# Kernel optimization log

Measured on AMD Instinct MI355X. Metric: run time of the kernel, lower is better.

Reference implementation:

```python
import jax, jax.numpy as jnp
import numpy as np

N_NODES = 50000


def _gcn_conv(x, src, dst, W, b, num_nodes):
    """PyG GCNConv: out = D^{-1/2}(A+I)D^{-1/2} (x @ W) + b, self-loops added."""
    h = x @ W  # [N, out]
    # degrees over edges incl. self-loops (src/dst already include self-loops)
    ones = jnp.ones(src.shape[0], dtype=h.dtype)
    deg = jax.ops.segment_sum(ones, dst, num_segments=num_nodes)
    dinv = jnp.where(deg > 0, jax.lax.rsqrt(deg), 0.0)
    norm = dinv[src] * dinv[dst]  # [E]
    msgs = h[src] * norm[:, None]  # [E, out] gather (memory-bound)
    out = jax.ops.segment_sum(msgs, dst, num_segments=num_nodes)
    return out + b


def setup_inputs() -> dict:
    key = jax.random.key(0)
    ks = jax.random.split(key, 8)
    in_c, h2, h1, out_c = 256, 256, 128, 128
    x = jax.random.normal(ks[0], (N_NODES, in_c), dtype=jnp.float32)
    edge_index = jax.random.randint(ks[1], (2, 800000), 0, N_NODES, dtype=jnp.int64)
    def glorot(k, fi, fo):
        s = float(np.sqrt(6.0 / (fi + fo)))
        return jax.random.uniform(k, (fi, fo), jnp.float32, -s, s)
    return {
        "x": x,
        "edge_index": edge_index,
        "W1": glorot(ks[2], in_c, h2), "b1": jnp.zeros((h2,), jnp.float32),
        "W2": glorot(ks[3], h2, h1), "b2": jnp.zeros((h1,), jnp.float32),
        "W3": glorot(ks[4], h1, out_c), "b3": jnp.zeros((out_c,), jnp.float32),
    }


def reference(x, edge_index, W1, b1, W2, b2, W3, b3):
    n = x.shape[0]
    loops = jnp.arange(n, dtype=edge_index.dtype)
    src = jnp.concatenate([edge_index[0], loops])
    dst = jnp.concatenate([edge_index[1], loops])
    # dropout is a no-op in eval mode (training=False)
    h1 = jax.nn.relu(_gcn_conv(x, src, dst, W1, b1, n))
    h2 = jax.nn.relu(_gcn_conv(h1, src, dst, W2, b2, n))
    h3 = jax.nn.relu(_gcn_conv(h2, src, dst, W3, b3, n))
    return jnp.concatenate([h1, h2, h3], axis=1)
```

## Files before the change

### kernel.cpp

```cpp
#include <hip/hip_runtime.h>

typedef __attribute__((ext_vector_type(8))) short bfrag8;
typedef __attribute__((ext_vector_type(4))) float f32x4v;

__device__ inline short f2bf(float f) {
    unsigned u = __builtin_bit_cast(unsigned, f);
    u = (u + 0x7FFFu + ((u >> 16) & 1u)) >> 16;
    return (short)u;
}
__device__ inline float bf2f(short s) {
    unsigned u = ((unsigned)(unsigned short)s) << 16;
    return __builtin_bit_cast(float, u);
}
__device__ inline int pack2(short lo, short hi) {
    return (int)(((unsigned)(unsigned short)lo) | (((unsigned)(unsigned short)hi) << 16));
}
__device__ inline void gload_lds16(const short* g, short* l) {
    __builtin_amdgcn_global_load_lds(
        (const __attribute__((address_space(1))) void*)g,
        (__attribute__((address_space(3))) void*)l, 16, 0, 0);
}


__global__ void deg_count_kernel(const int* __restrict__ dst, int E, int* __restrict__ deg) {
    int e = blockIdx.x * blockDim.x + threadIdx.x;
    if (e < E) atomicAdd(&deg[dst[e]], 1);
}

__global__ void block_sum_kernel(const int* __restrict__ deg, int n, int* __restrict__ bsums) {
    int i = blockIdx.x * 256 + threadIdx.x;
    int v = (i < n) ? deg[i] : 0;
#pragma unroll
    for (int off = 32; off > 0; off >>= 1) v += __shfl_down(v, off);
    __shared__ int wsum[4];
    int lane = threadIdx.x & 63, w = threadIdx.x >> 6;
    if (lane == 0) wsum[w] = v;
    __syncthreads();
    if (threadIdx.x == 0) bsums[blockIdx.x] = wsum[0] + wsum[1] + wsum[2] + wsum[3];
}

__global__ void scan_bsums_kernel(int* __restrict__ bsums, int B, int* __restrict__ offs, int n) {
    __shared__ int s[256];
    int tid = threadIdx.x;
    int v = (tid < B) ? bsums[tid] : 0;
    s[tid] = v;
    __syncthreads();
    for (int off = 1; off < 256; off <<= 1) {
        int t = (tid >= off) ? s[tid - off] : 0;
        __syncthreads();
        s[tid] += t;
        __syncthreads();
    }
    if (tid < B) bsums[tid] = (tid == 0) ? 0 : s[tid - 1];
    if (tid == 0) offs[n] = s[255];
}

__global__ void scan_final_kernel(const int* __restrict__ deg, int n,
                                  const int* __restrict__ bsums,
                                  int* __restrict__ offs, int* __restrict__ cursor,
                                  float* __restrict__ dinv) {
    __shared__ int s[256];
    int tid = threadIdx.x;
    int i = blockIdx.x * 256 + tid;
    int v = (i < n) ? deg[i] : 0;
    s[tid] = v;
    __syncthreads();
    for (int off = 1; off < 256; off <<= 1) {
        int t = (tid >= off) ? s[tid - off] : 0;
        __syncthreads();
        s[tid] += t;
        __syncthreads();
    }
    if (i < n) {
        int excl = s[tid] - v + bsums[blockIdx.x];
        offs[i] = excl;
        cursor[i] = excl;
        dinv[i] = rsqrtf((float)(v + 1));
    }
}

__global__ void csr_fill_kernel(const int* __restrict__ src, const int* __restrict__ dst, int E,
                                int* __restrict__ cursor, int* __restrict__ csr) {
    int e = blockIdx.x * blockDim.x + threadIdx.x;
    if (e < E) {
        int d = dst[e];
        int p = atomicAdd(&cursor[d], 1);
        csr[p] = src[e];
    }
}


__global__ void wt_kernel(const float* __restrict__ W, short* __restrict__ Wt,
                          int K, int logN) {
    int i = blockIdx.x * blockDim.x + threadIdx.x;
    int total = K << logN;
    if (i < total) {
        int k = i >> logN;
        int n = i & ((1 << logN) - 1);
        Wt[(size_t)n * K + k] = f2bf(W[i]);
    }
}


__global__ void x2b_kernel(const float* __restrict__ x, short* __restrict__ xb, int total8) {
    int i = blockIdx.x * blockDim.x + threadIdx.x;
    if (i < total8) {
        const float4* p = (const float4*)(x + (size_t)i * 8);
        float4 v0 = p[0], v1 = p[1];
        int4 w = make_int4(pack2(f2bf(v0.x), f2bf(v0.y)), pack2(f2bf(v0.z), f2bf(v0.w)),
                           pack2(f2bf(v1.x), f2bf(v1.y)), pack2(f2bf(v1.z), f2bf(v1.w)));
        *(int4*)(xb + (size_t)i * 8) = w;
    }
}


__global__ __launch_bounds__(256) void gemm_bf16_kernel(
        const short* __restrict__ A, int lda,
        const short* __restrict__ Bt, int K,
        const float* __restrict__ dinv,
        short* __restrict__ Tout, int ldt,
        int M) {
    __shared__ short As[128 * 32];
    __shared__ short Bs[128 * 32];

    const int tid = threadIdx.x;
    const int lane = tid & 63;
    const int wid = tid >> 6;
    const int l15 = lane & 15;
    const int quad = lane >> 4;
    const int q8 = quad * 8;
    const int bm = blockIdx.x * 128;
    const int bn = blockIdx.y * 128;
    const int wm = (wid & 1) * 64;
    const int wn = (wid >> 1) * 64;

    f32x4v acc[4][4];
#pragma unroll
    for (int i = 0; i < 4; ++i)
#pragma unroll
        for (int j = 0; j < 4; ++j) acc[i][j] = (f32x4v){0.f, 0.f, 0.f, 0.f};

    const int f0 = wid * 2048 + lane * 16;
    const int r0 = f0 >> 6, c0 = (f0 & 63) >> 1;
    const int f1 = f0 + 1024;
    const int r1 = f1 >> 6, c1 = (f1 & 63) >> 1;
    short* ldsA = As + wid * 1024;
    short* ldsB = Bs + wid * 1024;

    const short* a0 = A + (size_t)(bm + r0) * lda + c0;
    const short* a1 = A + (size_t)(bm + r1) * lda + c1;
    const short* b0 = Bt + (size_t)(bn + r0) * K + c0;
    const short* b1 = Bt + (size_t)(bn + r1) * K + c1;

    for (int k0 = 0; k0 < K; k0 += 32) {
        gload_lds16(a0 + k0, ldsA);
        gload_lds16(a1 + k0, ldsA + 512);
        gload_lds16(b0 + k0, ldsB);
        gload_lds16(b1 + k0, ldsB + 512);
        __syncthreads();

        bfrag8 af[4], bfv[4];
#pragma unroll
        for (int mt = 0; mt < 4; ++mt)
            af[mt] = *(const bfrag8*)&As[(wm + mt * 16 + l15) * 32 + q8];
#pragma unroll
        for (int nt = 0; nt < 4; ++nt)
            bfv[nt] = *(const bfrag8*)&Bs[(wn + nt * 16 + l15) * 32 + q8];
#pragma unroll
        for (int mt = 0; mt < 4; ++mt)
#pragma unroll
            for (int nt = 0; nt < 4; ++nt)
                acc[mt][nt] = __builtin_amdgcn_mfma_f32_16x16x32_bf16(af[mt], bfv[nt], acc[mt][nt], 0, 0, 0);
        __syncthreads();
    }

#pragma unroll
    for (int mt = 0; mt < 4; ++mt) {
#pragma unroll
        for (int r = 0; r < 4; ++r) {
            int grow = bm + wm + mt * 16 + quad * 4 + r;
            if (grow < M) {
                float di = dinv[grow];
                short* outp = Tout + (size_t)grow * ldt + bn + wn + l15;
#pragma unroll
                for (int nt = 0; nt < 4; ++nt)
                    outp[nt * 16] = f2bf(acc[mt][nt][r] * di);
            }
        }
    }
}


template<int C, bool WB>
__global__ __launch_bounds__(256) void agg_kernel(
        const short* __restrict__ hn, const float* __restrict__ dinv,
        const int* __restrict__ offs, const int* __restrict__ csr,
        const float* __restrict__ bias, float* __restrict__ out,
        short* __restrict__ hb, int coloff, int n) {
    constexpr int V = C / 64;
    int node = blockIdx.x * 4 + (threadIdx.x >> 6);
    if (node >= n) return;
    int lane = threadIdx.x & 63;
    const short* base = hn + lane * V;

    float acc[V];
#pragma unroll
    for (int v = 0; v < V; ++v) acc[v] = 0.f;

    int beg = offs[node], end = offs[node + 1];
    int e = beg;
    if (V == 4) {
        for (; e + 8 <= end; e += 8) {
            short4 r[8];
#pragma unroll
            for (int j = 0; j < 8; ++j)
                r[j] = *(const short4*)(base + (size_t)csr[e + j] * C);
#pragma unroll
            for (int j = 0; j < 8; ++j) {
                acc[0] += bf2f(r[j].x); acc[1] += bf2f(r[j].y);
                acc[2] += bf2f(r[j].z); acc[3] += bf2f(r[j].w);
            }
        }
        for (; e < end; ++e) {
            short4 a = *(const short4*)(base + (size_t)csr[e] * C);
            acc[0] += bf2f(a.x); acc[1] += bf2f(a.y); acc[2] += bf2f(a.z); acc[3] += bf2f(a.w);
        }
        short4 a = *(const short4*)(base + (size_t)node * C);
        acc[0] += bf2f(a.x); acc[1] += bf2f(a.y); acc[2] += bf2f(a.z); acc[3] += bf2f(a.w);
    } else {
        for (; e + 8 <= end; e += 8) {
            short2 r[8];
#pragma unroll
            for (int j = 0; j < 8; ++j)
                r[j] = *(const short2*)(base + (size_t)csr[e + j] * C);
#pragma unroll
            for (int j = 0; j < 8; ++j) {
                acc[0] += bf2f(r[j].x); acc[1] += bf2f(r[j].y);
            }
        }
        for (; e < end; ++e) {
            short2 a = *(const short2*)(base + (size_t)csr[e] * C);
            acc[0] += bf2f(a.x); acc[1] += bf2f(a.y);
        }
        short2 a = *(const short2*)(base + (size_t)node * C);
        acc[0] += bf2f(a.x); acc[1] += bf2f(a.y);
    }

    float di = dinv[node];
    float res[V];
#pragma unroll
    for (int v = 0; v < V; ++v)
        res[v] = fmaxf(fmaf(di, acc[v], bias[lane * V + v]), 0.f);

    float* op = out + (size_t)node * 512 + coloff + lane * V;
    if (V == 4) {
        *(float4*)op = make_float4(res[0], res[1], res[2], res[3]);
        if (WB) {
            int2 w = make_int2(pack2(f2bf(res[0]), f2bf(res[1])), pack2(f2bf(res[2]), f2bf(res[3])));
            *(int2*)(hb + (size_t)node * C + lane * V) = w;
        }
    } else {
        *(float2*)op = make_float2(res[0], res[1]);
        if (WB) {
            *(int*)(hb + (size_t)node * C + lane * V) = pack2(f2bf(res[0]), f2bf(res[1]));
        }
    }
}


extern "C" void kernel_launch(void* const* d_in, const int* in_sizes, int n_in,
                              void* d_out, int out_size, void* d_ws, size_t ws_size,
                              hipStream_t stream) {
    const float* x  = (const float*)d_in[0];
    const int*   ei = (const int*)d_in[1];
    const float* W1 = (const float*)d_in[2];
    const float* b1 = (const float*)d_in[3];
    const float* W2 = (const float*)d_in[4];
    const float* b2 = (const float*)d_in[5];
    const float* W3 = (const float*)d_in[6];
    const float* b3 = (const float*)d_in[7];

    const int IN_C = 256, H2 = 256, H1 = 128, OUT_C = 128;
    int n = in_sizes[0] / IN_C;
    int E = in_sizes[1] / 2;
    const int* src = ei;
    const int* dst = ei + E;

    int mb = (n + 127) / 128;
    int npad = mb * 128;

    char* ws = (char*)d_ws;
    auto carve = [&](size_t bytes) { char* p = ws; ws += (bytes + 255) & ~(size_t)255; return p; };
    int*   deg    = (int*)  carve((size_t)n * 4);
    int*   offs   = (int*)  carve(((size_t)n + 1) * 4);
    int*   cursor = (int*)  carve((size_t)n * 4);
    float* dinv   = (float*)carve((size_t)n * 4);
    int*   csr    = (int*)  carve((size_t)E * 4);
    int*   bsums  = (int*)  carve(256 * 4);
    short* Wt1    = (short*)carve((size_t)IN_C * H2 * 2);
    short* Wt2    = (short*)carve((size_t)H2 * H1 * 2);
    short* Wt3    = (short*)carve((size_t)H1 * OUT_C * 2);
    short* t      = (short*)carve((size_t)npad * 256 * 2);
    short* inb    = (short*)carve((size_t)npad * 256 * 2);

    float* out = (float*)d_out;
    int nblk = (n + 255) / 256;

    hipMemsetAsync(deg, 0, (size_t)n * sizeof(int), stream);
    deg_count_kernel<<<(E + 255) / 256, 256, 0, stream>>>(dst, E, deg);
    block_sum_kernel<<<nblk, 256, 0, stream>>>(deg, n, bsums);
    scan_bsums_kernel<<<1, 256, 0, stream>>>(bsums, nblk, offs, n);
    scan_final_kernel<<<nblk, 256, 0, stream>>>(deg, n, bsums, offs, cursor, dinv);
    csr_fill_kernel<<<(E + 255) / 256, 256, 0, stream>>>(src, dst, E, cursor, csr);

    wt_kernel<<<(IN_C * H2 + 255) / 256, 256, 0, stream>>>(W1, Wt1, IN_C, 8);
    wt_kernel<<<(H2 * H1 + 255) / 256, 256, 0, stream>>>(W2, Wt2, H2, 7);
    wt_kernel<<<(H1 * OUT_C + 255) / 256, 256, 0, stream>>>(W3, Wt3, H1, 7);

    int total8 = n * IN_C / 8;
    x2b_kernel<<<(total8 + 255) / 256, 256, 0, stream>>>(x, inb, total8);

    gemm_bf16_kernel<<<dim3(mb, H2 / 128), 256, 0, stream>>>(inb, IN_C, Wt1, IN_C, dinv, t, H2, n);
    agg_kernel<256, true><<<(n + 3) / 4, 256, 0, stream>>>(t, dinv, offs, csr, b1, out, inb, 0, n);

    gemm_bf16_kernel<<<dim3(mb, H1 / 128), 256, 0, stream>>>(inb, H2, Wt2, H2, dinv, t, H1, n);
    agg_kernel<128, true><<<(n + 3) / 4, 256, 0, stream>>>(t, dinv, offs, csr, b2, out, inb, H2, n);

    gemm_bf16_kernel<<<dim3(mb, OUT_C / 128), 256, 0, stream>>>(inb, H1, Wt3, H1, dinv, t, OUT_C, n);
    agg_kernel<128, false><<<(n + 3) / 4, 256, 0, stream>>>(t, dinv, offs, csr, b3, out, nullptr, H2 + H1, n);
}
```

Baseline: 445.2 us.

## Replace tiled bf16 GEMM with skinny GEMM keeping full weight slice in LDS

The k-looped 128x128 GEMM, which staged both A and B through LDS with two barriers per k-step, is replaced by a kernel templated on K. Each block loads a padded 64-column weight slice into LDS once, and each wave reads its A fragments directly from global memory across the fully unrolled K loop. This removes the per-iteration barriers and the A staging, and uses a padded LDS stride to avoid bank conflicts. In exchange, A is read from global without coalescing through LDS, A rows are re-read once per 64-column slice, and the M bounds check is dropped. The dinv and workspace buffers are padded to 256-row multiples, so the tail rows read unset dinv values and write into padding.

```diff
diff --git a/kernel.cpp b/kernel.cpp
--- a/kernel.cpp
+++ b/kernel.cpp
@@ -14,11 +14,6 @@
 }
 __device__ inline int pack2(short lo, short hi) {
     return (int)(((unsigned)(unsigned short)lo) | (((unsigned)(unsigned short)hi) << 16));
-}
-__device__ inline void gload_lds16(const short* g, short* l) {
-    __builtin_amdgcn_global_load_lds(
-        (const __attribute__((address_space(1))) void*)g,
-        (__attribute__((address_space(3))) void*)l, 16, 0, 0);
 }
 
 
@@ -114,14 +109,14 @@
 }
 
 
-__global__ __launch_bounds__(256) void gemm_bf16_kernel(
-        const short* __restrict__ A, int lda,
-        const short* __restrict__ Bt, int K,
+template<int K>
+__global__ __launch_bounds__(256, 2) void gemm_skinny_kernel(
+        const short* __restrict__ A,
+        const short* __restrict__ Bt,
         const float* __restrict__ dinv,
-        short* __restrict__ Tout, int ldt,
-        int M) {
-    __shared__ short As[128 * 32];
-    __shared__ short Bs[128 * 32];
+        short* __restrict__ Tout, int ldt) {
+    constexpr int BSTR = K + 8;
+    __shared__ short Bs[64 * BSTR];
 
     const int tid = threadIdx.x;
     const int lane = tid & 63;
@@ -129,10 +124,19 @@
     const int l15 = lane & 15;
     const int quad = lane >> 4;
     const int q8 = quad * 8;
-    const int bm = blockIdx.x * 128;
-    const int bn = blockIdx.y * 128;
-    const int wm = (wid & 1) * 64;
-    const int wn = (wid >> 1) * 64;
+    const int bn = blockIdx.y * 64;
+    const int row0 = blockIdx.x * 256 + wid * 64;
+
+    {
+        constexpr int TOT16 = 64 * K / 8;
+#pragma unroll
+        for (int i = tid; i < TOT16; i += 256) {
+            int r = i / (K / 8);
+            int c = (i % (K / 8)) * 8;
+            *(int4*)&Bs[r * BSTR + c] = *(const int4*)&Bt[(size_t)(bn + r) * K + c];
+        }
+    }
+    __syncthreads();
 
     f32x4v acc[4][4];
 #pragma unroll
@@ -140,52 +144,34 @@
 #pragma unroll
         for (int j = 0; j < 4; ++j) acc[i][j] = (f32x4v){0.f, 0.f, 0.f, 0.f};
 
-    const int f0 = wid * 2048 + lane * 16;
-    const int r0 = f0 >> 6, c0 = (f0 & 63) >> 1;
-    const int f1 = f0 + 1024;
-    const int r1 = f1 >> 6, c1 = (f1 & 63) >> 1;
-    short* ldsA = As + wid * 1024;
-    short* ldsB = Bs + wid * 1024;
-
-    const short* a0 = A + (size_t)(bm + r0) * lda + c0;
-    const short* a1 = A + (size_t)(bm + r1) * lda + c1;
-    const short* b0 = Bt + (size_t)(bn + r0) * K + c0;
-    const short* b1 = Bt + (size_t)(bn + r1) * K + c1;
-
-    for (int k0 = 0; k0 < K; k0 += 32) {
-        gload_lds16(a0 + k0, ldsA);
-        gload_lds16(a1 + k0, ldsA + 512);
-        gload_lds16(b0 + k0, ldsB);
-        gload_lds16(b1 + k0, ldsB + 512);
-        __syncthreads();
-
-        bfrag8 af[4], bfv[4];
+    const short* aBase = A + (size_t)(row0 + l15) * K + q8;
+
+#pragma unroll
+    for (int ks = 0; ks < K / 32; ++ks) {
+        bfrag8 af[4], bf[4];
 #pragma unroll
         for (int mt = 0; mt < 4; ++mt)
-            af[mt] = *(const bfrag8*)&As[(wm + mt * 16 + l15) * 32 + q8];
+            af[mt] = *(const bfrag8*)(aBase + (size_t)mt * 16 * K + ks * 32);
 #pragma unroll
         for (int nt = 0; nt < 4; ++nt)
-            bfv[nt] = *(const bfrag8*)&Bs[(wn + nt * 16 + l15) * 32 + q8];
+            bf[nt] = *(const bfrag8*)&Bs[(nt * 16 + l15) * BSTR + ks * 32 + q8];
 #pragma unroll
         for (int mt = 0; mt < 4; ++mt)
 #pragma unroll
             for (int nt = 0; nt < 4; ++nt)
-                acc[mt][nt] = __builtin_amdgcn_mfma_f32_16x16x32_bf16(af[mt], bfv[nt], acc[mt][nt], 0, 0, 0);
-        __syncthreads();
+                acc[mt][nt] = __builtin_amdgcn_mfma_f32_16x16x32_bf16(af[mt], bf[nt], acc[mt][nt], 0, 0, 0);
     }
 
 #pragma unroll
     for (int mt = 0; mt < 4; ++mt) {
 #pragma unroll
         for (int r = 0; r < 4; ++r) {
-            int grow = bm + wm + mt * 16 + quad * 4 + r;
-            if (grow < M) {
-                float di = dinv[grow];
-                short* outp = Tout + (size_t)grow * ldt + bn + wn + l15;
-#pragma unroll
-                for (int nt = 0; nt < 4; ++nt)
-                    outp[nt * 16] = f2bf(acc[mt][nt][r] * di);
-            }
+            int grow = row0 + mt * 16 + quad * 4 + r;
+            float di = dinv[grow];
+            short* outp = Tout + (size_t)grow * ldt + bn + l15;
+#pragma unroll
+            for (int nt = 0; nt < 4; ++nt)
+                outp[nt * 16] = f2bf(acc[mt][nt][r] * di);
         }
     }
 }
@@ -286,15 +272,15 @@
     const int* src = ei;
     const int* dst = ei + E;
 
-    int mb = (n + 127) / 128;
-    int npad = mb * 128;
+    int sb = (n + 255) / 256;
+    int npad = sb * 256;
 
     char* ws = (char*)d_ws;
     auto carve = [&](size_t bytes) { char* p = ws; ws += (bytes + 255) & ~(size_t)255; return p; };
     int*   deg    = (int*)  carve((size_t)n * 4);
     int*   offs   = (int*)  carve(((size_t)n + 1) * 4);
     int*   cursor = (int*)  carve((size_t)n * 4);
-    float* dinv   = (float*)carve((size_t)n * 4);
+    float* dinv   = (float*)carve((size_t)npad * 4);
     int*   csr    = (int*)  carve((size_t)E * 4);
     int*   bsums  = (int*)  carve(256 * 4);
     short* Wt1    = (short*)carve((size_t)IN_C * H2 * 2);
@@ -320,12 +306,12 @@
     int total8 = n * IN_C / 8;
     x2b_kernel<<<(total8 + 255) / 256, 256, 0, stream>>>(x, inb, total8);
 
-    gemm_bf16_kernel<<<dim3(mb, H2 / 128), 256, 0, stream>>>(inb, IN_C, Wt1, IN_C, dinv, t, H2, n);
+    gemm_skinny_kernel<256><<<dim3(sb, H2 / 64), 256, 0, stream>>>(inb, Wt1, dinv, t, H2);
     agg_kernel<256, true><<<(n + 3) / 4, 256, 0, stream>>>(t, dinv, offs, csr, b1, out, inb, 0, n);
 
-    gemm_bf16_kernel<<<dim3(mb, H1 / 128), 256, 0, stream>>>(inb, H2, Wt2, H2, dinv, t, H1, n);
+    gemm_skinny_kernel<256><<<dim3(sb, H1 / 64), 256, 0, stream>>>(inb, Wt2, dinv, t, H1);
     agg_kernel<128, true><<<(n + 3) / 4, 256, 0, stream>>>(t, dinv, offs, csr, b2, out, inb, H2, n);
 
-    gemm_bf16_kernel<<<dim3(mb, OUT_C / 128), 256, 0, stream>>>(inb, H1, Wt3, H1, dinv, t, OUT_C, n);
+    gemm_skinny_kernel<128><<<dim3(sb, OUT_C / 64), 256, 0, stream>>>(inb, Wt3, dinv, t, OUT_C);
     agg_kernel<128, false><<<(n + 3) / 4, 256, 0, stream>>>(t, dinv, offs, csr, b3, out, nullptr, H2 + H1, n);
 }
```

After: 443.1 us. Within noise of the previous version (-0.5%).
